# Optimization experiments

Hardware: AMD Instinct MI355X
Metric: run time of the kernel (lower is better)

## Reference

```python
import jax, jax.numpy as jnp
import numpy as np

NUM_HEADS = 8
DIM_V = 128
LN_EPS = 1e-5


def _ln(x, g, b):
    m = jnp.mean(x, axis=-1, keepdims=True)
    v = jnp.var(x, axis=-1, keepdims=True)
    return (x - m) * jax.lax.rsqrt(v + LN_EPS) * g + b


def _gcn(x, adj_norm, W, b):
    # DenseGCNConv: out = D^-1/2 (A+I) D^-1/2 (x W) + b
    return jnp.einsum('bnm,bmf->bnf', adj_norm, x @ W) + b


def setup_inputs() -> dict:
    key = jax.random.key(0)
    ks = jax.random.split(key, 24)
    B, N, D = 8, 1024, 128
    Hd = NUM_HEADS * DIM_V  # 1024
    s = lambda fan: 1.0 / np.sqrt(fan)
    inp = {
        'H': jax.random.normal(ks[0], (B, N, D), jnp.float32),
        'A': jax.random.uniform(ks[1], (B, N, N), jnp.float32),
        'W_Q': jax.random.normal(ks[2], (D, Hd), jnp.float32) * s(D),
        'b_Q': jnp.zeros((Hd,), jnp.float32),
        'W_K': jax.random.normal(ks[3], (D, Hd), jnp.float32) * s(D),
        'b_K': jnp.zeros((Hd,), jnp.float32),
        'W_V': jax.random.normal(ks[4], (D, Hd), jnp.float32) * s(D),
        'b_V': jnp.zeros((Hd,), jnp.float32),
        'B_bias': jax.random.normal(ks[5], (NUM_HEADS, N, N), jnp.float32) * 0.02,
        'W_O': jax.random.normal(ks[6], (Hd, D), jnp.float32) * s(Hd),
        'g0': jnp.ones((D,), jnp.float32), 'be0': jnp.zeros((D,), jnp.float32),
        'g1': jnp.ones((D,), jnp.float32), 'be1': jnp.zeros((D,), jnp.float32),
        'g2': jnp.ones((D,), jnp.float32), 'be2': jnp.zeros((D,), jnp.float32),
        'g3': jnp.ones((D,), jnp.float32), 'be3': jnp.zeros((D,), jnp.float32),
        'W1': jax.random.normal(ks[7], (D, D), jnp.float32) * s(D),
        'b1': jnp.zeros((D,), jnp.float32),
        'W2': jax.random.normal(ks[8], (D, D), jnp.float32) * s(D),
        'b2': jnp.zeros((D,), jnp.float32),
    }
    return inp


def reference(H, A, W_Q, b_Q, W_K, b_K, W_V, b_V, B_bias, W_O,
              g0, be0, g1, be1, g2, be2, g3, be3, W1, b1, W2, b2):
    B, N, D = H.shape
    dk_scale = 1.0 / np.sqrt(np.float32(D))  # sqrt(dim_K)

    residual = H
    Hn = _ln(H, g0, be0)  # norm_type 'sw': pre-norm

    # GCN adjacency normalization with self-loops (shared by Q/K/V layers)
    I = jnp.eye(N, dtype=A.dtype)
    Ahat = A * (1.0 - I) + I
    dis = jax.lax.rsqrt(jnp.maximum(Ahat.sum(-1), 1.0))  # [B,N]
    adj_norm = dis[:, :, None] * Ahat * dis[:, None, :]

    Q = _gcn(Hn, adj_norm, W_Q, b_Q)  # [B,N,H*dV]
    K = _gcn(Hn, adj_norm, W_K, b_K)
    V = _gcn(Hn, adj_norm, W_V, b_V)

    # split heads: feature slice h*dV:(h+1)*dV -> head h
    Q_ = Q.reshape(B, N, NUM_HEADS, DIM_V).transpose(0, 2, 1, 3)
    K_ = K.reshape(B, N, NUM_HEADS, DIM_V).transpose(0, 2, 1, 3)
    V_ = V.reshape(B, N, NUM_HEADS, DIM_V).transpose(0, 2, 1, 3)

    scores = jnp.einsum('bhnd,bhmd->bhnm', Q_, K_) * dk_scale
    scores = scores + B_bias[None]  # 'BL': blended with learned per-head bias
    attn = jax.nn.softmax(scores, axis=-1)
    MH = jnp.einsum('bhnm,bhmd->bhnd', attn, V_)  # [B,H,N,dV]

    MH = _ln(MH, g1, be1)  # 'sw' GN1

    # concat heads back to features
    MHc = MH.transpose(0, 2, 1, 3).reshape(B, N, NUM_HEADS * DIM_V)
    O = MHc @ W_O + residual
    O = _ln(O, g2, be2)

    RO = jax.nn.relu(jax.nn.relu(O @ W1 + b1) @ W2 + b2)
    RO = _ln(RO, g3, be3)  # 'sw' GN3
    return O + RO
```

## Files before the change

kernel.cpp:

```cpp
#include <hip/hip_runtime.h>
#include <hip/hip_bf16.h>
#include <stdint.h>

typedef __attribute__((ext_vector_type(8))) short bf16x8;
typedef __attribute__((ext_vector_type(4))) short s16x4;
typedef __attribute__((ext_vector_type(4))) float f32x4;

__device__ __forceinline__ float bf2f(short s) {
    union { float f; uint32_t u; } v; v.u = ((uint32_t)(uint16_t)s) << 16; return v.f;
}
__device__ __forceinline__ short f2bf(float f) {
    union { float f; uint32_t u; } v; v.f = f;
    uint32_t u = v.u;
    u += 0x7FFFu + ((u >> 16) & 1u);
    return (short)(u >> 16);
}
__device__ __forceinline__ void gload_lds16(const void* g, void* l) {
    __builtin_amdgcn_global_load_lds(
        (const __attribute__((address_space(1))) uint32_t*)g,
        (__attribute__((address_space(3))) uint32_t*)l, 16, 0, 0);
}

template<int MODE>
__global__ __launch_bounds__(256) void ln_kernel(
    const float* __restrict__ x, const float* __restrict__ res,
    const float* __restrict__ gamma, const float* __restrict__ beta,
    float* __restrict__ outf, short* __restrict__ outb)
{
    const int row = blockIdx.x * 4 + (threadIdx.x >> 6);
    const int lane = threadIdx.x & 63;
    const long base = (long)row * 128;
    float2 v;
    if (MODE == 1) {
        v.x = 0.f; v.y = 0.f;
#pragma unroll
        for (int p = 0; p < 4; ++p) {
            float2 t = *(const float2*)(x + (long)p * 1048576 + base + lane * 2);
            v.x += t.x; v.y += t.y;
        }
        float2 rr = *(const float2*)(res + base + lane * 2);
        v.x += rr.x; v.y += rr.y;
    } else {
        v = *(const float2*)(x + base + lane * 2);
    }
    float s = v.x + v.y, s2 = v.x * v.x + v.y * v.y;
#pragma unroll
    for (int o = 32; o; o >>= 1) { s += __shfl_xor(s, o); s2 += __shfl_xor(s2, o); }
    const float mean = s * (1.f / 128.f);
    const float var = s2 * (1.f / 128.f) - mean * mean;
    const float rs = rsqrtf(var + 1e-5f);
    const float y0 = (v.x - mean) * rs * gamma[lane * 2] + beta[lane * 2];
    const float y1 = (v.y - mean) * rs * gamma[lane * 2 + 1] + beta[lane * 2 + 1];
    if (MODE == 0 || MODE == 1) {
        uint32_t pk = (uint32_t)(uint16_t)f2bf(y0) | ((uint32_t)(uint16_t)f2bf(y1) << 16);
        *(uint32_t*)(outb + base + lane * 2) = pk;
    }
    if (MODE == 1) {
        float2 o2; o2.x = y0; o2.y = y1;
        *(float2*)(outf + base + lane * 2) = o2;
    }
    if (MODE == 2) {
        float2 rr = *(const float2*)(res + base + lane * 2);
        float2 o2; o2.x = y0 + rr.x; o2.y = y1 + rr.y;
        *(float2*)(outf + base + lane * 2) = o2;
    }
}

__global__ __launch_bounds__(256) void dis_kernel(const float* __restrict__ A, float* __restrict__ dis)
{
    const int bn = blockIdx.x;
    const int n = bn & 1023;
    float4 v = ((const float4*)(A + (long)bn * 1024))[threadIdx.x];
    float s = v.x + v.y + v.z + v.w;
    if ((n >> 2) == (int)threadIdx.x) {
        s += 1.f - ((const float*)&v)[n & 3];
    }
#pragma unroll
    for (int o = 32; o; o >>= 1) s += __shfl_xor(s, o);
    __shared__ float red[4];
    if ((threadIdx.x & 63) == 0) red[threadIdx.x >> 6] = s;
    __syncthreads();
    if (threadIdx.x == 0) {
        float t = red[0] + red[1] + red[2] + red[3];
        dis[bn] = rsqrtf(fmaxf(t, 1.f));
    }
}

__global__ __launch_bounds__(256) void adjnorm_kernel(
    const float* __restrict__ A, const float* __restrict__ dis, short* __restrict__ adj)
{
    const int bn = blockIdx.x;
    const int b = bn >> 10, n = bn & 1023;
    const float dn = dis[bn];
    float4 v = ((const float4*)(A + (long)bn * 1024))[threadIdx.x];
    const int m0 = threadIdx.x * 4;
    const float* dm = dis + b * 1024 + m0;
    s16x4 o;
#pragma unroll
    for (int j = 0; j < 4; ++j) {
        float av = (m0 + j == n) ? 1.f : ((const float*)&v)[j];
        o[j] = f2bf(av * dn * dm[j]);
    }
    *(s16x4*)(adj + (long)bn * 1024 + m0) = o;
}

__global__ __launch_bounds__(256) void bconv_kernel(const float* __restrict__ Bb, short* __restrict__ bb)
{
    const long i = ((long)blockIdx.x * 256 + threadIdx.x) * 4;
    float4 v = *(const float4*)(Bb + i);
    s16x4 o; o[0] = f2bf(v.x); o[1] = f2bf(v.y); o[2] = f2bf(v.z); o[3] = f2bf(v.w);
    *(s16x4*)(bb + i) = o;
}

__global__ __launch_bounds__(256) void convw_kernel(
    const float* __restrict__ WQ, const float* __restrict__ WK, const float* __restrict__ WV,
    const float* __restrict__ bQ, const float* __restrict__ bK, const float* __restrict__ bV,
    const float* __restrict__ WO, const float* __restrict__ W1, const float* __restrict__ W2,
    short* __restrict__ WqkvT, float* __restrict__ bqkv, short* __restrict__ WoT,
    short* __restrict__ W1T, short* __restrict__ W2T)
{
    const int id = blockIdx.x * 256 + threadIdx.x;
    if (id < 393216) {
        const int f = id >> 7, k = id & 127;
        const float* W = (f < 1024) ? WQ : (f < 2048 ? WK : WV);
        WqkvT[id] = f2bf(W[k * 1024 + (f & 1023)]);
    } else if (id < 396288) {
        const int f = id - 393216;
        const float* bb = (f < 1024) ? bQ : (f < 2048 ? bK : bV);
        bqkv[f] = bb[f & 1023];
    } else if (id < 527360) {
        const int t = id - 396288;
        const int j = t >> 10, i = t & 1023;
        WoT[t] = f2bf(WO[i * 128 + j]);
    } else if (id < 543744) {
        const int t = id - 527360;
        W1T[t] = f2bf(W1[(t & 127) * 128 + (t >> 7)]);
    } else if (id < 560128) {
        const int t = id - 543744;
        W2T[t] = f2bf(W2[(t & 127) * 128 + (t >> 7)]);
    }
}

__global__ __launch_bounds__(256) void hntrans_kernel(const short* __restrict__ Hn, short* __restrict__ HnT)
{
    const int b = blockIdx.z;
    const int m0 = blockIdx.x * 64, f0 = blockIdx.y * 64;
    __shared__ short T[64][72];
    const int row = threadIdx.x >> 2;
    const int c = (threadIdx.x & 3) * 16;
    const short* src = Hn + (long)(b * 1024 + m0 + row) * 128 + f0 + c;
    *(bf16x8*)&T[row][c] = *(const bf16x8*)src;
    *(bf16x8*)&T[row][c + 8] = *(const bf16x8*)(src + 8);
    __syncthreads();
    short* dst = HnT + ((long)b * 128 + f0 + row) * 1024 + m0 + c;
    bf16x8 o0, o1;
#pragma unroll
    for (int i = 0; i < 8; ++i) { o0[i] = T[c + i][row]; o1[i] = T[c + 8 + i][row]; }
    *(bf16x8*)dst = o0;
    *(bf16x8*)(dst + 8) = o1;
}

__global__ __launch_bounds__(256) void ahred_kernel(const float* __restrict__ AHp, short* __restrict__ AH)
{
    const long i = ((long)blockIdx.x * 256 + threadIdx.x) * 4;
    const int b = (int)(i >> 17);
    const long r = i & 131071;
    const float* p = AHp + (long)b * 524288 + r;
    float4 v0 = *(const float4*)p;
    float4 v1 = *(const float4*)(p + 131072);
    float4 v2 = *(const float4*)(p + 262144);
    float4 v3 = *(const float4*)(p + 393216);
    s16x4 o;
    o[0] = f2bf(v0.x + v1.x + v2.x + v3.x);
    o[1] = f2bf(v0.y + v1.y + v2.y + v3.y);
    o[2] = f2bf(v0.z + v1.z + v2.z + v3.z);
    o[3] = f2bf(v0.w + v1.w + v2.w + v3.w);
    *(s16x4*)(AH + i) = o;
}

__global__ __launch_bounds__(256) void vtrans_kernel(const short* __restrict__ QKV, short* __restrict__ VT)
{
    const int bh = blockIdx.z, b = bh >> 3, h = bh & 7;
    const int n0 = blockIdx.x * 64, d0 = blockIdx.y * 64;
    __shared__ short T[64][72];
    const int row = threadIdx.x >> 2;
    const int c = (threadIdx.x & 3) * 16;
    const short* src = QKV + (long)(b * 1024 + n0 + row) * 3072 + 2048 + h * 128 + d0 + c;
    *(bf16x8*)&T[row][c] = *(const bf16x8*)src;
    *(bf16x8*)&T[row][c + 8] = *(const bf16x8*)(src + 8);
    __syncthreads();
    short* dst = VT + (long)(bh * 128 + d0 + row) * 1024 + n0 + c;
    bf16x8 o0, o1;
#pragma unroll
    for (int i = 0; i < 8; ++i) { o0[i] = T[c + i][row]; o1[i] = T[c + 8 + i][row]; }
    *(bf16x8*)dst = o0;
    *(bf16x8*)(dst + 8) = o1;
}

template<int BIAS_MODE, bool RELU, bool OUT_BF16>
__global__ __launch_bounds__(256) void gemm_kernel(
    const short* __restrict__ A, const short* __restrict__ Bt,
    const float* __restrict__ bias, void* __restrict__ Cv,
    int K, int lda, int ldb, int ldc,
    long batchA, long batchB, long batchC)
{
    __shared__ __align__(16) short Asm[128 * 32];
    __shared__ __align__(16) short Bsm[128 * 32];
    const int tid = threadIdx.x, lane = tid & 63, wave = tid >> 6;
    const int li = lane & 15, g = lane >> 4;
    const int mt = blockIdx.y * 128, nt = blockIdx.x * 128;
    A += (long)blockIdx.z * batchA;
    Bt += (long)blockIdx.z * batchB;

    const int wr = (wave >> 1) * 64, wc = (wave & 1) * 64;
    f32x4 acc[4][4] = {};

    const int srow = lane >> 2;
    const int scol = (lane & 3) * 8;
    const long aoff0 = (long)(mt + wave * 32 + srow) * lda + scol;
    const long aoff1 = aoff0 + (long)16 * lda;
    const long boff0 = (long)(nt + wave * 32 + srow) * ldb + scol;
    const long boff1 = boff0 + (long)16 * ldb;
    short* ad0 = &Asm[wave * 1024];
    short* ad1 = &Asm[wave * 1024 + 512];
    short* bd0 = &Bsm[wave * 1024];
    short* bd1 = &Bsm[wave * 1024 + 512];

    for (int k0 = 0; k0 < K; k0 += 32) {
        gload_lds16(A + aoff0 + k0, ad0);
        gload_lds16(A + aoff1 + k0, ad1);
        gload_lds16(Bt + boff0 + k0, bd0);
        gload_lds16(Bt + boff1 + k0, bd1);
        __syncthreads();
        bf16x8 af[4], bf[4];
#pragma unroll
        for (int m = 0; m < 4; ++m) af[m] = *(const bf16x8*)&Asm[(wr + m * 16 + li) * 32 + g * 8];
#pragma unroll
        for (int n = 0; n < 4; ++n) bf[n] = *(const bf16x8*)&Bsm[(wc + n * 16 + li) * 32 + g * 8];
#pragma unroll
        for (int m = 0; m < 4; ++m)
#pragma unroll
            for (int n = 0; n < 4; ++n)
                acc[m][n] = __builtin_amdgcn_mfma_f32_16x16x32_bf16(af[m], bf[n], acc[m][n], 0, 0, 0);
        __syncthreads();
    }

    const long cbase = (long)blockIdx.z * batchC;
#pragma unroll
    for (int m = 0; m < 4; ++m) {
        const int row0 = mt + wr + m * 16 + g * 4;
#pragma unroll
        for (int n = 0; n < 4; ++n) {
            const int col = nt + wc + n * 16 + li;
            float bc = (BIAS_MODE == 1) ? bias[col] : 0.f;
#pragma unroll
            for (int r = 0; r < 4; ++r) {
                float x = acc[m][n][r] + bc;
                if (RELU) x = fmaxf(x, 0.f);
                const long idx = cbase + (long)(row0 + r) * ldc + col;
                if (OUT_BF16) ((short*)Cv)[idx] = f2bf(x);
                else          ((float*)Cv)[idx] = x;
            }
        }
    }
}

template<int BIAS_MODE, bool RELU, bool OUT_BF16, int KSPLIT = 1>
__global__ __launch_bounds__(256) void gemm64_kernel(
    const short* __restrict__ A, const short* __restrict__ Bt,
    const float* __restrict__ bias, void* __restrict__ Cv,
    int K, int lda, int ldb, int ldc,
    long batchA, long batchB, long batchC)
{
    __shared__ __align__(16) short Asm[64 * 32];
    __shared__ __align__(16) short Bsm[64 * 32];
    const int tid = threadIdx.x, lane = tid & 63, wave = tid >> 6;
    const int li = lane & 15, g = lane >> 4;
    const int mt = blockIdx.y * 64, nt = blockIdx.x * 64;
    const int wr = (wave >> 1) * 32, wc = (wave & 1) * 32;
    const int zb = blockIdx.z / KSPLIT;
    const int kc = blockIdx.z % KSPLIT;
    A += (long)zb * batchA + (long)kc * K;
    Bt += (long)zb * batchB + (long)kc * K;
    f32x4 acc[2][2] = {};

    const int srow = lane >> 2;
    const int scol = (lane & 3) * 8;
    const long aoff = (long)(mt + wave * 16 + srow) * lda + scol;
    const long boff = (long)(nt + wave * 16 + srow) * ldb + scol;

    for (int k0 = 0; k0 < K; k0 += 32) {
        gload_lds16(A + aoff + k0, &Asm[wave * 512]);
        gload_lds16(Bt + boff + k0, &Bsm[wave * 512]);
        __syncthreads();
        bf16x8 af[2], bf[2];
#pragma unroll
        for (int m = 0; m < 2; ++m) af[m] = *(const bf16x8*)&Asm[(wr + m * 16 + li) * 32 + g * 8];
#pragma unroll
        for (int n = 0; n < 2; ++n) bf[n] = *(const bf16x8*)&Bsm[(wc + n * 16 + li) * 32 + g * 8];
#pragma unroll
        for (int m = 0; m < 2; ++m)
#pragma unroll
            for (int n = 0; n < 2; ++n)
                acc[m][n] = __builtin_amdgcn_mfma_f32_16x16x32_bf16(af[m], bf[n], acc[m][n], 0, 0, 0);
        __syncthreads();
    }

    const long cbase = (long)blockIdx.z * batchC;
#pragma unroll
    for (int m = 0; m < 2; ++m) {
        const int row0 = mt + wr + m * 16 + g * 4;
#pragma unroll
        for (int n = 0; n < 2; ++n) {
            const int col = nt + wc + n * 16 + li;
            float bc = (BIAS_MODE == 1) ? bias[col] : 0.f;
#pragma unroll
            for (int r = 0; r < 4; ++r) {
                float x = acc[m][n][r] + bc;
                if (RELU) x = fmaxf(x, 0.f);
                const long idx = cbase + (long)(row0 + r) * ldc + col;
                if (OUT_BF16) ((short*)Cv)[idx] = f2bf(x);
                else          ((float*)Cv)[idx] = x;
            }
        }
    }
}

__global__ __launch_bounds__(512, 2) void attn_kernel(
    const short* __restrict__ QKV, const short* __restrict__ VT,
    const short* __restrict__ biasb,
    const float* __restrict__ g1v, const float* __restrict__ be1v,
    short* __restrict__ MHc)
{
    const int tid = threadIdx.x;
    const int lane = tid & 63;
    const int wave = tid >> 6;
    const int li = lane & 15;
    const int g = lane >> 4;

    const int id = blockIdx.x;
    const int h = id & 7;
    const int b = (id >> 3) & 7;
    const int qt = id >> 6;
    const int q0 = qt * 128;

    __shared__ __align__(16) short Ksm[64 * 128];
    __shared__ __align__(16) short Vsm[128 * 64];
    __shared__ __align__(16) short Psm[8][16 * 72];

    bf16x8 qf[4];
    {
        const short* Qb = QKV + ((long)(b * 1024 + q0 + wave * 16 + li) * 3072 + h * 128);
#pragma unroll
        for (int dc = 0; dc < 4; ++dc)
            qf[dc] = *(const bf16x8*)(Qb + dc * 32 + g * 8);
    }

    float ll[4];
#pragma unroll
    for (int r = 0; r < 4; ++r) ll[r] = 0.f;
    f32x4 oacc[8] = {};

    const long kbase = (long)(b * 1024) * 3072 + 1024 + h * 128;
    const int kr0 = wave * 8 + g;
    const int kc0 = ((li * 16) ^ ((kr0 & 7) << 4)) >> 1;
    const int kc1 = ((li * 16) ^ (((kr0 + 4) & 7) << 4)) >> 1;
    const int vd_loc = lane >> 3;
    const int vcol = (((lane & 7) * 16) ^ (vd_loc << 4)) >> 1;
    const long vrowbase = ((long)(b * 8 + h) * 128) * 1024;

    const float scale = 0.08838834764831845f;
    const long bb_row0 = (long)h * 1024 + q0 + wave * 16 + g * 4;

    for (int kv0 = 0; kv0 < 1024; kv0 += 64) {
        gload_lds16(QKV + kbase + (long)(kv0 + kr0) * 3072 + kc0, &Ksm[wave * 1024]);
        gload_lds16(QKV + kbase + (long)(kv0 + kr0 + 4) * 3072 + kc1, &Ksm[wave * 1024 + 512]);
        gload_lds16(VT + vrowbase + (long)(wave * 16 + vd_loc) * 1024 + kv0 + vcol,
                    &Vsm[(wave * 16) * 64]);
        gload_lds16(VT + vrowbase + (long)(wave * 16 + 8 + vd_loc) * 1024 + kv0 + vcol,
                    &Vsm[(wave * 16 + 8) * 64]);
        __syncthreads();

        float bs[4][4];
#pragma unroll
        for (int r = 0; r < 4; ++r) {
            const short* bp = biasb + (bb_row0 + r) * 1024 + kv0 + li;
#pragma unroll
            for (int j = 0; j < 4; ++j)
                bs[r][j] = bf2f(bp[j * 16]);
        }

        const f32x4 fz = {0.f, 0.f, 0.f, 0.f};
        f32x4 sacc[4] = {fz, fz, fz, fz};
#pragma unroll
        for (int j = 0; j < 4; ++j) {
            const int r = j * 16 + li;
            const int sw = (r & 7) << 4;
#pragma unroll
            for (int dc = 0; dc < 4; ++dc) {
                bf16x8 kf = *(const bf16x8*)((const char*)Ksm + r * 256 + ((dc * 64 + g * 16) ^ sw));
                sacc[j] = __builtin_amdgcn_mfma_f32_16x16x32_bf16(qf[dc], kf, sacc[j], 0, 0, 0);
            }
        }

#pragma unroll
        for (int r = 0; r < 4; ++r) {
            short* pp = &Psm[wave][(g * 4 + r) * 72];
            float psum = 0.f;
#pragma unroll
            for (int j = 0; j < 4; ++j) {
                const float p = __expf(sacc[j][r] * scale + bs[r][j]);
                psum += p;
                pp[j * 16 + li] = f2bf(p);
            }
            ll[r] += psum;
        }

#pragma unroll
        for (int c = 0; c < 2; ++c) {
            bf16x8 pf = *(const bf16x8*)((const char*)&Psm[wave][0] + li * 144 + c * 64 + g * 16);
#pragma unroll
            for (int df = 0; df < 8; ++df) {
                bf16x8 vf = *(const bf16x8*)((const char*)Vsm + (df * 16 + li) * 128
                                             + ((c * 64 + g * 16) ^ ((li & 7) << 4)));
                oacc[df] = __builtin_amdgcn_mfma_f32_16x16x32_bf16(pf, vf, oacc[df], 0, 0, 0);
            }
        }
        __syncthreads();
    }

#pragma unroll
    for (int r = 0; r < 4; ++r) {
        const int qloc = g * 4 + r;
        float l = ll[r];
#pragma unroll
        for (int o = 1; o < 16; o <<= 1) l += __shfl_xor(l, o);
        const float inv = 1.f / l;
        float vals[8];
        float s1 = 0.f, s2 = 0.f;
#pragma unroll
        for (int df = 0; df < 8; ++df) {
            float v = oacc[df][r] * inv;
            vals[df] = v; s1 += v; s2 += v * v;
        }
#pragma unroll
        for (int o = 1; o < 16; o <<= 1) { s1 += __shfl_xor(s1, o); s2 += __shfl_xor(s2, o); }
        const float mean = s1 * (1.f / 128.f);
        const float var = s2 * (1.f / 128.f) - mean * mean;
        const float rs = rsqrtf(var + 1e-5f);
        const long orow = (long)(b * 1024 + q0 + wave * 16 + qloc) * 1024 + h * 128;
#pragma unroll
        for (int df = 0; df < 8; ++df) {
            const int d = df * 16 + li;
            MHc[orow + d] = f2bf((vals[df] - mean) * rs * g1v[d] + be1v[d]);
        }
    }
}

extern "C" void kernel_launch(void* const* d_in, const int* in_sizes, int n_in,
                              void* d_out, int out_size, void* d_ws, size_t ws_size,
                              hipStream_t stream)
{
    const float* H  = (const float*)d_in[0];
    const float* A  = (const float*)d_in[1];
    const float* WQ = (const float*)d_in[2];
    const float* bQ = (const float*)d_in[3];
    const float* WK = (const float*)d_in[4];
    const float* bK = (const float*)d_in[5];
    const float* WV = (const float*)d_in[6];
    const float* bV = (const float*)d_in[7];
    const float* Bb = (const float*)d_in[8];
    const float* WO = (const float*)d_in[9];
    const float* g0 = (const float*)d_in[10]; const float* be0 = (const float*)d_in[11];
    const float* g1 = (const float*)d_in[12]; const float* be1 = (const float*)d_in[13];
    const float* g2 = (const float*)d_in[14]; const float* be2 = (const float*)d_in[15];
    const float* g3 = (const float*)d_in[16]; const float* be3 = (const float*)d_in[17];
    const float* W1 = (const float*)d_in[18]; const float* b1 = (const float*)d_in[19];
    const float* W2 = (const float*)d_in[20]; const float* b2 = (const float*)d_in[21];
    float* out = (float*)d_out;

    char* ws = (char*)d_ws;
    short* Hn    = (short*)(ws + 0);
    short* adj   = (short*)(ws + 2097152);
    float* dis   = (float*)(ws + 18874368);
    short* WqkvT = (short*)(ws + 18907136);
    float* bqkv  = (float*)(ws + 19693568);
    short* WoT   = (short*)(ws + 19705856);
    short* W1T   = (short*)(ws + 19968000);
    short* W2T   = (short*)(ws + 20000768);
    short* biasb = (short*)(ws + 20033536);
    short* QKV   = (short*)(ws + 36810752);
    float* AHp   = (float*)(ws + 87142400);
    short* AH    = (short*)(ws + 103919616);
    short* HnT   = (short*)(ws + 106016768);
    short* VT    = adj;
    short* MHc   = (short*)(ws + 87142400);
    float* preO4 = (float*)(ws + 36810752);
    float* O     = (float*)(ws + 108113920);
    short* Obf   = (short*)(ws + 112308224);
    short* G1    = (short*)(ws + 114405376);
    float* G2    = (float*)(ws + 116502528);

    ln_kernel<0><<<2048, 256, 0, stream>>>(H, nullptr, g0, be0, nullptr, Hn);
    dis_kernel<<<8192, 256, 0, stream>>>(A, dis);
    adjnorm_kernel<<<8192, 256, 0, stream>>>(A, dis, adj);
    bconv_kernel<<<8192, 256, 0, stream>>>(Bb, biasb);
    convw_kernel<<<2188, 256, 0, stream>>>(WQ, WK, WV, bQ, bK, bV, WO, W1, W2,
                                           WqkvT, bqkv, WoT, W1T, W2T);
    hntrans_kernel<<<dim3(16, 2, 8), 256, 0, stream>>>(Hn, HnT);

    gemm64_kernel<0, false, false, 4><<<dim3(2, 16, 32), 256, 0, stream>>>(
        adj, HnT, nullptr, AHp, 256, 1024, 1024, 128,
        1048576L, 131072L, 131072L);
    ahred_kernel<<<1024, 256, 0, stream>>>(AHp, AH);

    gemm_kernel<1, false, true><<<dim3(24, 64, 1), 256, 0, stream>>>(
        AH, WqkvT, bqkv, QKV, 128, 128, 128, 3072, 0, 0, 0);

    vtrans_kernel<<<dim3(16, 2, 64), 256, 0, stream>>>(QKV, VT);
    attn_kernel<<<512, 512, 0, stream>>>(QKV, VT, biasb, g1, be1, MHc);

    gemm64_kernel<0, false, false, 4><<<dim3(2, 128, 4), 256, 0, stream>>>(
        MHc, WoT, nullptr, preO4, 256, 1024, 1024, 128, 0, 0, 1048576L);
    ln_kernel<1><<<2048, 256, 0, stream>>>(preO4, H, g2, be2, O, Obf);
    gemm64_kernel<1, true, true><<<dim3(2, 128, 1), 256, 0, stream>>>(
        Obf, W1T, b1, G1, 128, 128, 128, 128, 0, 0, 0);
    gemm64_kernel<1, true, false><<<dim3(2, 128, 1), 256, 0, stream>>>(
        G1, W2T, b2, G2, 128, 128, 128, 128, 0, 0, 0);
    ln_kernel<2><<<2048, 256, 0, stream>>>(G2, O, g3, be3, out, nullptr);
}
```

Before: 189.6 us.

## Merge prep kernels into two launches and halve split-K factor

Folds the LN0, degree, bias conversion and weight conversion kernels into one block-indexed prep kernel, and the adjacency normalization and Hn transpose into a second one, cutting the launch count. Both split-K GEMMs (adj·Hn and MHc·Wo) now use 2 K-splits of 512 instead of 4 of 256, and the reduction and LN kernels are changed to sum two partials. This cuts launch overhead and partial-sum traffic, at the cost of fewer blocks in the split-K GEMMs and less parallelism there.

```diff
diff --git a/kernel.cpp b/kernel.cpp
--- a/kernel.cpp
+++ b/kernel.cpp
@@ -34,7 +34,7 @@
     if (MODE == 1) {
         v.x = 0.f; v.y = 0.f;
 #pragma unroll
-        for (int p = 0; p < 4; ++p) {
+        for (int p = 0; p < 2; ++p) {
             float2 t = *(const float2*)(x + (long)p * 1048576 + base + lane * 2);
             v.x += t.x; v.y += t.y;
         }
@@ -66,98 +66,117 @@
     }
 }
 
-__global__ __launch_bounds__(256) void dis_kernel(const float* __restrict__ A, float* __restrict__ dis)
-{
-    const int bn = blockIdx.x;
-    const int n = bn & 1023;
-    float4 v = ((const float4*)(A + (long)bn * 1024))[threadIdx.x];
-    float s = v.x + v.y + v.z + v.w;
-    if ((n >> 2) == (int)threadIdx.x) {
-        s += 1.f - ((const float*)&v)[n & 3];
-    }
-#pragma unroll
-    for (int o = 32; o; o >>= 1) s += __shfl_xor(s, o);
-    __shared__ float red[4];
-    if ((threadIdx.x & 63) == 0) red[threadIdx.x >> 6] = s;
-    __syncthreads();
-    if (threadIdx.x == 0) {
-        float t = red[0] + red[1] + red[2] + red[3];
-        dis[bn] = rsqrtf(fmaxf(t, 1.f));
-    }
-}
-
-__global__ __launch_bounds__(256) void adjnorm_kernel(
-    const float* __restrict__ A, const float* __restrict__ dis, short* __restrict__ adj)
-{
-    const int bn = blockIdx.x;
-    const int b = bn >> 10, n = bn & 1023;
-    const float dn = dis[bn];
-    float4 v = ((const float4*)(A + (long)bn * 1024))[threadIdx.x];
-    const int m0 = threadIdx.x * 4;
-    const float* dm = dis + b * 1024 + m0;
-    s16x4 o;
-#pragma unroll
-    for (int j = 0; j < 4; ++j) {
-        float av = (m0 + j == n) ? 1.f : ((const float*)&v)[j];
-        o[j] = f2bf(av * dn * dm[j]);
-    }
-    *(s16x4*)(adj + (long)bn * 1024 + m0) = o;
-}
-
-__global__ __launch_bounds__(256) void bconv_kernel(const float* __restrict__ Bb, short* __restrict__ bb)
-{
-    const long i = ((long)blockIdx.x * 256 + threadIdx.x) * 4;
-    float4 v = *(const float4*)(Bb + i);
-    s16x4 o; o[0] = f2bf(v.x); o[1] = f2bf(v.y); o[2] = f2bf(v.z); o[3] = f2bf(v.w);
-    *(s16x4*)(bb + i) = o;
-}
-
-__global__ __launch_bounds__(256) void convw_kernel(
+__global__ __launch_bounds__(256) void prep1_kernel(
+    const float* __restrict__ H, const float* __restrict__ A, const float* __restrict__ Bb,
     const float* __restrict__ WQ, const float* __restrict__ WK, const float* __restrict__ WV,
     const float* __restrict__ bQ, const float* __restrict__ bK, const float* __restrict__ bV,
     const float* __restrict__ WO, const float* __restrict__ W1, const float* __restrict__ W2,
+    const float* __restrict__ g0, const float* __restrict__ be0,
+    short* __restrict__ Hn, float* __restrict__ dis, short* __restrict__ biasb,
     short* __restrict__ WqkvT, float* __restrict__ bqkv, short* __restrict__ WoT,
     short* __restrict__ W1T, short* __restrict__ W2T)
 {
-    const int id = blockIdx.x * 256 + threadIdx.x;
-    if (id < 393216) {
-        const int f = id >> 7, k = id & 127;
-        const float* W = (f < 1024) ? WQ : (f < 2048 ? WK : WV);
-        WqkvT[id] = f2bf(W[k * 1024 + (f & 1023)]);
-    } else if (id < 396288) {
-        const int f = id - 393216;
-        const float* bb = (f < 1024) ? bQ : (f < 2048 ? bK : bV);
-        bqkv[f] = bb[f & 1023];
-    } else if (id < 527360) {
-        const int t = id - 396288;
-        const int j = t >> 10, i = t & 1023;
-        WoT[t] = f2bf(WO[i * 128 + j]);
-    } else if (id < 543744) {
-        const int t = id - 527360;
-        W1T[t] = f2bf(W1[(t & 127) * 128 + (t >> 7)]);
-    } else if (id < 560128) {
-        const int t = id - 543744;
-        W2T[t] = f2bf(W2[(t & 127) * 128 + (t >> 7)]);
-    }
-}
-
-__global__ __launch_bounds__(256) void hntrans_kernel(const short* __restrict__ Hn, short* __restrict__ HnT)
-{
-    const int b = blockIdx.z;
-    const int m0 = blockIdx.x * 64, f0 = blockIdx.y * 64;
+    __shared__ float red[4];
+    const int id = blockIdx.x;
+    const int tid = threadIdx.x;
+    if (id < 2048) {
+        const int row = id * 4 + (tid >> 6);
+        const int lane = tid & 63;
+        const long base = (long)row * 128;
+        float2 v = *(const float2*)(H + base + lane * 2);
+        float s = v.x + v.y, s2 = v.x * v.x + v.y * v.y;
+#pragma unroll
+        for (int o = 32; o; o >>= 1) { s += __shfl_xor(s, o); s2 += __shfl_xor(s2, o); }
+        const float mean = s * (1.f / 128.f);
+        const float var = s2 * (1.f / 128.f) - mean * mean;
+        const float rs = rsqrtf(var + 1e-5f);
+        const float y0 = (v.x - mean) * rs * g0[lane * 2] + be0[lane * 2];
+        const float y1 = (v.y - mean) * rs * g0[lane * 2 + 1] + be0[lane * 2 + 1];
+        uint32_t pk = (uint32_t)(uint16_t)f2bf(y0) | ((uint32_t)(uint16_t)f2bf(y1) << 16);
+        *(uint32_t*)(Hn + base + lane * 2) = pk;
+    } else if (id < 10240) {
+        const int bn = id - 2048;
+        const int n = bn & 1023;
+        float4 v = ((const float4*)(A + (long)bn * 1024))[tid];
+        float s = v.x + v.y + v.z + v.w;
+        if ((n >> 2) == tid) {
+            s += 1.f - ((const float*)&v)[n & 3];
+        }
+#pragma unroll
+        for (int o = 32; o; o >>= 1) s += __shfl_xor(s, o);
+        if ((tid & 63) == 0) red[tid >> 6] = s;
+        __syncthreads();
+        if (tid == 0) {
+            float t = red[0] + red[1] + red[2] + red[3];
+            dis[bn] = rsqrtf(fmaxf(t, 1.f));
+        }
+    } else if (id < 18432) {
+        const long i = ((long)(id - 10240) * 256 + tid) * 4;
+        float4 v = *(const float4*)(Bb + i);
+        s16x4 o; o[0] = f2bf(v.x); o[1] = f2bf(v.y); o[2] = f2bf(v.z); o[3] = f2bf(v.w);
+        *(s16x4*)(biasb + i) = o;
+    } else {
+        const int gid = (id - 18432) * 256 + tid;
+        if (gid < 393216) {
+            const int f = gid >> 7, k = gid & 127;
+            const float* W = (f < 1024) ? WQ : (f < 2048 ? WK : WV);
+            WqkvT[gid] = f2bf(W[k * 1024 + (f & 1023)]);
+        } else if (gid < 396288) {
+            const int f = gid - 393216;
+            const float* bb = (f < 1024) ? bQ : (f < 2048 ? bK : bV);
+            bqkv[f] = bb[f & 1023];
+        } else if (gid < 527360) {
+            const int t = gid - 396288;
+            const int j = t >> 10, i = t & 1023;
+            WoT[t] = f2bf(WO[i * 128 + j]);
+        } else if (gid < 543744) {
+            const int t = gid - 527360;
+            W1T[t] = f2bf(W1[(t & 127) * 128 + (t >> 7)]);
+        } else if (gid < 560128) {
+            const int t = gid - 543744;
+            W2T[t] = f2bf(W2[(t & 127) * 128 + (t >> 7)]);
+        }
+    }
+}
+
+__global__ __launch_bounds__(256) void prep2_kernel(
+    const float* __restrict__ A, const float* __restrict__ dis, const short* __restrict__ Hn,
+    short* __restrict__ adj, short* __restrict__ HnT)
+{
     __shared__ short T[64][72];
-    const int row = threadIdx.x >> 2;
-    const int c = (threadIdx.x & 3) * 16;
-    const short* src = Hn + (long)(b * 1024 + m0 + row) * 128 + f0 + c;
-    *(bf16x8*)&T[row][c] = *(const bf16x8*)src;
-    *(bf16x8*)&T[row][c + 8] = *(const bf16x8*)(src + 8);
-    __syncthreads();
-    short* dst = HnT + ((long)b * 128 + f0 + row) * 1024 + m0 + c;
-    bf16x8 o0, o1;
-#pragma unroll
-    for (int i = 0; i < 8; ++i) { o0[i] = T[c + i][row]; o1[i] = T[c + 8 + i][row]; }
-    *(bf16x8*)dst = o0;
-    *(bf16x8*)(dst + 8) = o1;
+    const int id = blockIdx.x;
+    const int tid = threadIdx.x;
+    if (id < 8192) {
+        const int bn = id;
+        const int b = bn >> 10, n = bn & 1023;
+        const float dn = dis[bn];
+        float4 v = ((const float4*)(A + (long)bn * 1024))[tid];
+        const int m0 = tid * 4;
+        const float* dm = dis + b * 1024 + m0;
+        s16x4 o;
+#pragma unroll
+        for (int j = 0; j < 4; ++j) {
+            float av = (m0 + j == n) ? 1.f : ((const float*)&v)[j];
+            o[j] = f2bf(av * dn * dm[j]);
+        }
+        *(s16x4*)(adj + (long)bn * 1024 + m0) = o;
+    } else {
+        const int t = id - 8192;
+        const int bx = t & 15, by = (t >> 4) & 1, bz = t >> 5;
+        const int m0 = bx * 64, f0 = by * 64;
+        const int row = tid >> 2;
+        const int c = (tid & 3) * 16;
+        const short* src = Hn + (long)(bz * 1024 + m0 + row) * 128 + f0 + c;
+        *(bf16x8*)&T[row][c] = *(const bf16x8*)src;
+        *(bf16x8*)&T[row][c + 8] = *(const bf16x8*)(src + 8);
+        __syncthreads();
+        short* dst = HnT + ((long)bz * 128 + f0 + row) * 1024 + m0 + c;
+        bf16x8 o0, o1;
+#pragma unroll
+        for (int i = 0; i < 8; ++i) { o0[i] = T[c + i][row]; o1[i] = T[c + 8 + i][row]; }
+        *(bf16x8*)dst = o0;
+        *(bf16x8*)(dst + 8) = o1;
+    }
 }
 
 __global__ __launch_bounds__(256) void ahred_kernel(const float* __restrict__ AHp, short* __restrict__ AH)
@@ -165,16 +184,14 @@
     const long i = ((long)blockIdx.x * 256 + threadIdx.x) * 4;
     const int b = (int)(i >> 17);
     const long r = i & 131071;
-    const float* p = AHp + (long)b * 524288 + r;
+    const float* p = AHp + (long)b * 262144 + r;
     float4 v0 = *(const float4*)p;
     float4 v1 = *(const float4*)(p + 131072);
-    float4 v2 = *(const float4*)(p + 262144);
-    float4 v3 = *(const float4*)(p + 393216);
     s16x4 o;
-    o[0] = f2bf(v0.x + v1.x + v2.x + v3.x);
-    o[1] = f2bf(v0.y + v1.y + v2.y + v3.y);
-    o[2] = f2bf(v0.z + v1.z + v2.z + v3.z);
-    o[3] = f2bf(v0.w + v1.w + v2.w + v3.w);
+    o[0] = f2bf(v0.x + v1.x);
+    o[1] = f2bf(v0.y + v1.y);
+    o[2] = f2bf(v0.z + v1.z);
+    o[3] = f2bf(v0.w + v1.w);
     *(s16x4*)(AH + i) = o;
 }
 
@@ -501,16 +518,13 @@
     short* G1    = (short*)(ws + 114405376);
     float* G2    = (float*)(ws + 116502528);
 
-    ln_kernel<0><<<2048, 256, 0, stream>>>(H, nullptr, g0, be0, nullptr, Hn);
-    dis_kernel<<<8192, 256, 0, stream>>>(A, dis);
-    adjnorm_kernel<<<8192, 256, 0, stream>>>(A, dis, adj);
-    bconv_kernel<<<8192, 256, 0, stream>>>(Bb, biasb);
-    convw_kernel<<<2188, 256, 0, stream>>>(WQ, WK, WV, bQ, bK, bV, WO, W1, W2,
-                                           WqkvT, bqkv, WoT, W1T, W2T);
-    hntrans_kernel<<<dim3(16, 2, 8), 256, 0, stream>>>(Hn, HnT);
-
-    gemm64_kernel<0, false, false, 4><<<dim3(2, 16, 32), 256, 0, stream>>>(
-        adj, HnT, nullptr, AHp, 256, 1024, 1024, 128,
+    prep1_kernel<<<20620, 256, 0, stream>>>(H, A, Bb, WQ, WK, WV, bQ, bK, bV,
+                                            WO, W1, W2, g0, be0,
+                                            Hn, dis, biasb, WqkvT, bqkv, WoT, W1T, W2T);
+    prep2_kernel<<<8448, 256, 0, stream>>>(A, dis, Hn, adj, HnT);
+
+    gemm64_kernel<0, false, false, 2><<<dim3(2, 16, 16), 256, 0, stream>>>(
+        adj, HnT, nullptr, AHp, 512, 1024, 1024, 128,
         1048576L, 131072L, 131072L);
     ahred_kernel<<<1024, 256, 0, stream>>>(AHp, AH);
 
@@ -520,8 +534,8 @@
     vtrans_kernel<<<dim3(16, 2, 64), 256, 0, stream>>>(QKV, VT);
     attn_kernel<<<512, 512, 0, stream>>>(QKV, VT, biasb, g1, be1, MHc);
 
-    gemm64_kernel<0, false, false, 4><<<dim3(2, 128, 4), 256, 0, stream>>>(
-        MHc, WoT, nullptr, preO4, 256, 1024, 1024, 128, 0, 0, 1048576L);
+    gemm64_kernel<0, false, false, 2><<<dim3(2, 128, 2), 256, 0, stream>>>(
+        MHc, WoT, nullptr, preO4, 512, 1024, 1024, 128, 0, 0, 1048576L);
     ln_kernel<1><<<2048, 256, 0, stream>>>(preO4, H, g2, be2, O, Obf);
     gemm64_kernel<1, true, true><<<dim3(2, 128, 1), 256, 0, stream>>>(
         Obf, W1T, b1, G1, 128, 128, 128, 128, 0, 0, 0);
```

After: 163.6 us. 13.7% less time.
